# Optimization experiments

Hardware: AMD Instinct MI355X
Metric: run time of the kernel (lower is better)

Reference implementation:

```python
import jax, jax.numpy as jnp
import numpy as np

B, S, D, H = 2, 2048, 1024, 16
HD = D // H           # 64
AD = D // 8           # adapter dim 128


def setup_inputs() -> dict:
    key = jax.random.key(0)
    ks = jax.random.split(key, 16)
    s = 1.0 / np.sqrt(D)
    sa = 1.0 / np.sqrt(AD)
    return {
        "q": jax.random.normal(ks[0], (B, S, D), jnp.float32),
        "k": jax.random.normal(ks[1], (B, S, D), jnp.float32),
        "v": jax.random.normal(ks[2], (B, S, D), jnp.float32),
        "Wq": jax.random.normal(ks[3], (D, D), jnp.float32) * s,
        "bq": jnp.zeros((D,), jnp.float32),
        "Wk": jax.random.normal(ks[4], (D, D), jnp.float32) * s,
        "bk": jnp.zeros((D,), jnp.float32),
        "Wv": jax.random.normal(ks[5], (D, D), jnp.float32) * s,
        "bv": jnp.zeros((D,), jnp.float32),
        "Wo": jax.random.normal(ks[6], (D, D), jnp.float32) * s,
        "bo": jnp.zeros((D,), jnp.float32),
        "Wad": jax.random.normal(ks[7], (AD, D), jnp.float32) * s,
        "bad": jnp.zeros((AD,), jnp.float32),
        "Wau": jax.random.normal(ks[8], (D, AD), jnp.float32) * sa,
        "bau": jnp.zeros((D,), jnp.float32),
    }


def reference(q, k, v, Wq, bq, Wk, bk, Wv, bv, Wo, bo, Wad, bad, Wau, bau):
    # Linear projections (torch Linear: x @ W.T + b), split into heads
    def proj(x, W, b):
        y = jnp.einsum('bsd,ed->bse', x, W) + b
        return y.reshape(B, -1, H, HD).transpose(0, 2, 1, 3)  # [B,H,S,HD]

    qh, kh, vh = proj(q, Wq, bq), proj(k, Wk, bk), proj(v, Wv, bv)
    scores = jnp.einsum('bhqd,bhkd->bhqk', qh, kh) / np.sqrt(HD)  # [B,H,S,S]
    attn = jax.nn.softmax(scores, axis=-1)
    ctx = jnp.einsum('bhqk,bhkd->bhqd', attn, vh)
    ctx = ctx.transpose(0, 2, 1, 3).reshape(B, -1, D)  # [B,S,D]
    out = jnp.einsum('bsd,ed->bse', ctx, Wo) + bo
    # adapter: down -> GELU (exact erf) -> up, fused with residual
    a = jnp.einsum('bsd,ad->bsa', out, Wad) + bad
    a = jax.nn.gelu(a, approximate=False)
    a = jnp.einsum('bsa,da->bsd', a, Wau) + bau
    return out + a
```

## Files before the change

kernel.cpp:

```cpp
#include <hip/hip_runtime.h>
#include <hip/hip_bf16.h>
#include <math.h>

typedef __attribute__((ext_vector_type(8))) short short8;
typedef __attribute__((ext_vector_type(4))) float f32x4;

#define MFMA16(a,b,c) __builtin_amdgcn_mfma_f32_16x16x32_bf16((a),(b),(c),0,0,0)

__device__ __forceinline__ unsigned short f2bf(float f){
    union { __hip_bfloat16 b; unsigned short u; } cv;
    cv.b = __float2bfloat16(f);
    return cv.u;
}
__device__ __forceinline__ unsigned pk_bf16(float a, float b){
    unsigned r;
    asm("v_cvt_pk_bf16_f32 %0, %1, %2" : "=v"(r) : "v"(a), "v"(b));
    return r;
}
__device__ __forceinline__ float ex2(float x){
    return __builtin_amdgcn_exp2f(x);
}

#define GLD_LDS16(g, s) \
    __builtin_amdgcn_global_load_lds((const __attribute__((address_space(1))) void*)(g), \
                                     (__attribute__((address_space(3))) void*)(s), 16, 0, 0)

#define QSCALE 0.18033688011112042f
#define DEFER_THR 11.0f

struct CvtJobs {
    const float* src[9];
    unsigned short* dst[9];
    float scale[9];
    int n[9];
};

__global__ __launch_bounds__(256)
void convert_kernel(CvtJobs j, long long total4) {
    long long i4 = (long long)blockIdx.x * blockDim.x + threadIdx.x;
    if (i4 >= total4) return;
    long long rem = i4 * 4;
    int job = 0;
    while (job < 9 && rem >= j.n[job]) { rem -= j.n[job]; ++job; }
    if (job >= 9) return;
    const float sc = j.scale[job];
    const float4 v = *(const float4*)(j.src[job] + rem);
    ushort4 o;
    o.x = f2bf(v.x * sc); o.y = f2bf(v.y * sc);
    o.z = f2bf(v.z * sc); o.w = f2bf(v.w * sc);
    *(ushort4*)(j.dst[job] + rem) = o;
}

#define GEMM128_LOOP(Aptr, Bptr)                                                     \
    f32x4 acc[4][4] = {};                                                            \
    for (int k0 = 0; k0 < K; k0 += 32) {                                             \
        __syncthreads();                                                             \
        _Pragma("unroll")                                                            \
        for (int c = 0; c < 2; ++c) {                                                \
            const int id = c * 256 + tid;                                            \
            const int row = id >> 2, u = id & 3;                                     \
            const int su = u ^ ((row >> 1) & 3);                                     \
            GLD_LDS16((const char*)(Aptr) + ((size_t)(m0 + row) * K + k0) * 2 + su * 16, \
                      (char*)As + (c * 256 + w * 64) * 16);                          \
            GLD_LDS16((const char*)(Bptr) + ((size_t)(n0 + row) * K + k0) * 2 + su * 16, \
                      (char*)Bs + (c * 256 + w * 64) * 16);                          \
        }                                                                            \
        __syncthreads();                                                             \
        short8 af[4], bfr[4];                                                        \
        _Pragma("unroll")                                                            \
        for (int i = 0; i < 4; ++i)                                                  \
            af[i] = *(const short8*)((const char*)As + (wr * 64 + i * 16 + lr) * 64 + ru * 16); \
        _Pragma("unroll")                                                            \
        for (int jj = 0; jj < 4; ++jj)                                               \
            bfr[jj] = *(const short8*)((const char*)Bs + (wc * 64 + jj * 16 + lr) * 64 + ru * 16); \
        _Pragma("unroll")                                                            \
        for (int i = 0; i < 4; ++i)                                                  \
            _Pragma("unroll")                                                        \
            for (int jj = 0; jj < 4; ++jj)                                           \
                acc[i][jj] = MFMA16(af[i], bfr[jj], acc[i][jj]);                     \
    }

struct QKVArgs {
    const unsigned short* A[3];
    const unsigned short* W[3];
    const float* bias[3];
    float bscale[3];
    unsigned short* out[3];
};

__global__ __launch_bounds__(256)
void gemm_qkv(QKVArgs ar, int M, int N, int K)
{
    __shared__ unsigned short As[128 * 32];
    __shared__ unsigned short Bs[128 * 32];

    const int z = blockIdx.z;
    const unsigned short* A = ar.A[z];
    const unsigned short* W = ar.W[z];
    const int tid = threadIdx.x;
    const int w = tid >> 6, l = tid & 63;
    const int lr = l & 15, lg = l >> 4;
    const int wr = w >> 1, wc = w & 1;
    const int m0 = blockIdx.x * 128, n0 = blockIdx.y * 128;
    const int ru = lg ^ ((lr >> 1) & 3);

    GEMM128_LOOP(A, W)

    const float* bias = ar.bias[z];
    const float bsc = ar.bscale[z];
    unsigned short* out = ar.out[z];
    #pragma unroll
    for (int i = 0; i < 4; ++i)
        #pragma unroll
        for (int jj = 0; jj < 4; ++jj)
            #pragma unroll
            for (int r = 0; r < 4; ++r) {
                const int row = m0 + wr * 64 + i * 16 + lg * 4 + r;
                const int col = n0 + wc * 64 + jj * 16 + lr;
                const float c = acc[i][jj][r] + bias[col] * bsc;
                const int b = row >> 11, s = row & 2047, h = col >> 6, hd = col & 63;
                if (z < 2)
                    out[((((size_t)(b * 16 + h)) * 2048 + s) << 6) + hd] = f2bf(c);
                else
                    out[((((size_t)(b * 16 + h)) * 64 + hd) << 11) + s] = f2bf(c);
            }
}

template<int MODE>
__global__ __launch_bounds__(256)
void gemm_bf16(const unsigned short* __restrict__ A,
               const unsigned short* __restrict__ Wt,
               const float* __restrict__ bias,
               void* __restrict__ out0,
               void* __restrict__ out1,
               int M, int N, int K)
{
    __shared__ unsigned short As[128 * 32];
    __shared__ unsigned short Bs[128 * 32];

    const int tid = threadIdx.x;
    const int w = tid >> 6, l = tid & 63;
    const int lr = l & 15, lg = l >> 4;
    const int wr = w >> 1, wc = w & 1;
    const int m0 = blockIdx.x * 128, n0 = blockIdx.y * 128;
    const int ru = lg ^ ((lr >> 1) & 3);

    GEMM128_LOOP(A, Wt)

    #pragma unroll
    for (int i = 0; i < 4; ++i)
        #pragma unroll
        for (int jj = 0; jj < 4; ++jj)
            #pragma unroll
            for (int r = 0; r < 4; ++r) {
                const int row = m0 + wr * 64 + i * 16 + lg * 4 + r;
                const int col = n0 + wc * 64 + jj * 16 + lr;
                const float c = acc[i][jj][r] + bias[col];
                if (MODE == 2) {
                    ((float*)out0)[(size_t)row * N + col] = c;
                    ((unsigned short*)out1)[(size_t)row * N + col] = f2bf(c);
                } else {
                    ((float*)out0)[(size_t)row * N + col] =
                        c + ((const float*)out1)[(size_t)row * N + col];
                }
            }
}

__global__ __launch_bounds__(256)
void gemm64_gelu(const unsigned short* __restrict__ A,
                 const unsigned short* __restrict__ Wt,
                 const float* __restrict__ bias,
                 unsigned short* __restrict__ out,
                 int M, int N, int K)
{
    __shared__ unsigned short As[64 * 32];
    __shared__ unsigned short Bs[64 * 32];

    const int tid = threadIdx.x;
    const int w = tid >> 6, l = tid & 63;
    const int lr = l & 15, lg = l >> 4;
    const int wr = w >> 1, wc = w & 1;
    const int m0 = blockIdx.x * 64, n0 = blockIdx.y * 64;

    f32x4 acc[2][2] = {};

    for (int k0 = 0; k0 < K; k0 += 32) {
        const int row = tid >> 2, ch = tid & 3;
        __syncthreads();
        GLD_LDS16(A  + (size_t)(m0 + row) * K + k0 + ch * 8, As + (w * 64) * 8);
        GLD_LDS16(Wt + (size_t)(n0 + row) * K + k0 + ch * 8, Bs + (w * 64) * 8);
        __syncthreads();

        short8 af[2], bfr[2];
        #pragma unroll
        for (int i = 0; i < 2; ++i)
            af[i] = *(const short8*)(As + ((wr * 32 + i * 16 + lr) * 32 + lg * 8));
        #pragma unroll
        for (int jj = 0; jj < 2; ++jj)
            bfr[jj] = *(const short8*)(Bs + ((wc * 32 + jj * 16 + lr) * 32 + lg * 8));
        #pragma unroll
        for (int i = 0; i < 2; ++i)
            #pragma unroll
            for (int jj = 0; jj < 2; ++jj)
                acc[i][jj] = MFMA16(af[i], bfr[jj], acc[i][jj]);
    }

    #pragma unroll
    for (int i = 0; i < 2; ++i)
        #pragma unroll
        for (int jj = 0; jj < 2; ++jj)
            #pragma unroll
            for (int r = 0; r < 4; ++r) {
                const int row = m0 + wr * 32 + i * 16 + lg * 4 + r;
                const int col = n0 + wc * 32 + jj * 16 + lr;
                const float c = acc[i][jj][r] + bias[col];
                const float g = 0.5f * c * (1.0f + erff(c * 0.70710678118654752f));
                out[(size_t)row * N + col] = f2bf(g);
            }
}

__global__ __launch_bounds__(256)
void attn_mfma(const unsigned short* __restrict__ Qh,
               const unsigned short* __restrict__ Kh,
               const unsigned short* __restrict__ Vt,
               unsigned short* __restrict__ ctx)
{
    __shared__ unsigned short Ks[2][64 * 64];
    __shared__ unsigned short Vs[2][64 * 64];
    __shared__ unsigned short Ps[4][32 * 64];

    const int tid = threadIdx.x;
    const int w = tid >> 6, l = tid & 63;
    const int lr = l & 15, lg = l >> 4;

    const int p = blockIdx.x + blockIdx.y * 16;
    const int id = (p & 7) * 64 + (p >> 3);
    const int q0 = (id & 15) << 7;
    const int bh = id >> 4;

    const unsigned short* Qb = Qh + (size_t)bh * 131072;
    const char* Kb = (const char*)(Kh + (size_t)bh * 131072);
    const char* Vb = (const char*)(Vt + (size_t)bh * 131072);

    short8 qf[2][2];
    #pragma unroll
    for (int mm = 0; mm < 2; ++mm)
        #pragma unroll
        for (int c = 0; c < 2; ++c)
            qf[mm][c] = *(const short8*)(Qb + (size_t)(q0 + w * 32 + mm * 16 + lr) * 64
                                            + c * 32 + lg * 8);

    float mrow[2] = {-1e30f, -1e30f};
    float lrow[2] = {0.f, 0.f};
    f32x4 accO[2][4] = {};

    auto STAGE = [&](int bf, int kt) {
        #pragma unroll
        for (int c = 0; c < 2; ++c) {
            const int cid = c * 256 + tid;
            const int row = cid >> 3, u = cid & 7;
            const int su = u ^ (row & 7);
            GLD_LDS16(Kb + (size_t)(kt + row) * 128 + su * 16,
                      (char*)&Ks[bf][0] + (c * 256 + w * 64) * 16);
            GLD_LDS16(Vb + (size_t)row * 4096 + (size_t)kt * 2 + su * 16,
                      (char*)&Vs[bf][0] + (c * 256 + w * 64) * 16);
        }
    };

    STAGE(0, 0);
    __syncthreads();

    int cur = 0;
    for (int t = 0; t < 32; ++t) {
        if (t < 31) STAGE(cur ^ 1, (t + 1) * 64);

        const char* Kbuf = (const char*)&Ks[cur][0];
        const char* Vbuf = (const char*)&Vs[cur][0];

        f32x4 sf[2][4] = {};
        #pragma unroll
        for (int n = 0; n < 4; ++n) {
            const int krow = n * 16 + lr;
            const short8 kf0 = *(const short8*)(Kbuf + krow * 128 + ((0 * 4 + lg) ^ (lr & 7)) * 16);
            const short8 kf1 = *(const short8*)(Kbuf + krow * 128 + ((1 * 4 + lg) ^ (lr & 7)) * 16);
            #pragma unroll
            for (int mm = 0; mm < 2; ++mm) {
                sf[mm][n] = MFMA16(kf0, qf[mm][0], sf[mm][n]);
                sf[mm][n] = MFMA16(kf1, qf[mm][1], sf[mm][n]);
            }
        }

        short8 vf[4][2];
        #pragma unroll
        for (int n = 0; n < 4; ++n) {
            const int drow = n * 16 + lr;
            vf[n][0] = *(const short8*)(Vbuf + drow * 128 + ((0 * 4 + lg) ^ (lr & 7)) * 16);
            vf[n][1] = *(const short8*)(Vbuf + drow * 128 + ((1 * 4 + lg) ^ (lr & 7)) * 16);
        }

        float rm[2];
        bool need = false;
        #pragma unroll
        for (int mm = 0; mm < 2; ++mm) {
            float a = fmaxf(fmaxf(fmaxf(sf[mm][0][0], sf[mm][0][1]),
                                  fmaxf(sf[mm][0][2], sf[mm][0][3])),
                            fmaxf(fmaxf(sf[mm][1][0], sf[mm][1][1]),
                                  fmaxf(sf[mm][1][2], sf[mm][1][3])));
            float b = fmaxf(fmaxf(fmaxf(sf[mm][2][0], sf[mm][2][1]),
                                  fmaxf(sf[mm][2][2], sf[mm][2][3])),
                            fmaxf(fmaxf(sf[mm][3][0], sf[mm][3][1]),
                                  fmaxf(sf[mm][3][2], sf[mm][3][3])));
            float r2 = fmaxf(a, b);
            r2 = fmaxf(r2, __shfl_xor(r2, 16));
            r2 = fmaxf(r2, __shfl_xor(r2, 32));
            rm[mm] = r2;
            need |= (r2 > mrow[mm] + DEFER_THR);
        }
        if (__any(need)) {
            #pragma unroll
            for (int mm = 0; mm < 2; ++mm) {
                const float mnew = fmaxf(mrow[mm], rm[mm]);
                const float rsc = ex2(mrow[mm] - mnew);
                lrow[mm] *= rsc;
                mrow[mm] = mnew;
                #pragma unroll
                for (int r = 0; r < 4; ++r) {
                    const float rr = __shfl(rsc, (l & 48) | (lg * 4 + r));
                    #pragma unroll
                    for (int n = 0; n < 4; ++n) accO[mm][n][r] *= rr;
                }
            }
        }
        #pragma unroll
        for (int mm = 0; mm < 2; ++mm) {
            const float m = mrow[mm];
            float ls = lrow[mm];
            char* pbase = (char*)&Ps[w][0] + (mm * 16 + lr) * 128;
            #pragma unroll
            for (int n = 0; n < 4; ++n) {
                const float p0 = ex2(sf[mm][n][0] - m);
                const float p1 = ex2(sf[mm][n][1] - m);
                const float p2 = ex2(sf[mm][n][2] - m);
                const float p3 = ex2(sf[mm][n][3] - m);
                ls += (p0 + p1) + (p2 + p3);
                uint2 pk;
                pk.x = pk_bf16(p0, p1);
                pk.y = pk_bf16(p2, p3);
                *(uint2*)(pbase + (((n * 2 + (lg >> 1)) ^ (lr & 7)) * 16) + (lg & 1) * 8) = pk;
            }
            lrow[mm] = ls;
        }

        asm volatile("" ::: "memory");

        short8 pf[2][2];
        #pragma unroll
        for (int mm = 0; mm < 2; ++mm) {
            const char* pb = (const char*)&Ps[w][0] + (mm * 16 + lr) * 128;
            #pragma unroll
            for (int c = 0; c < 2; ++c) {
                union { uint2 q2[2]; short8 s8; } cvt;
                const char* base = pb + (((c * 4 + lg) ^ (lr & 7)) * 16);
                cvt.q2[0] = *(const uint2*)(base);
                cvt.q2[1] = *(const uint2*)(base + 8);
                pf[mm][c] = cvt.s8;
            }
        }

        #pragma unroll
        for (int n = 0; n < 4; ++n) {
            #pragma unroll
            for (int mm = 0; mm < 2; ++mm) {
                accO[mm][n] = MFMA16(pf[mm][0], vf[n][0], accO[mm][n]);
                accO[mm][n] = MFMA16(pf[mm][1], vf[n][1], accO[mm][n]);
            }
        }

        __syncthreads();
        cur ^= 1;
    }

    const int b = bh >> 4, h = bh & 15;
    #pragma unroll
    for (int mm = 0; mm < 2; ++mm) {
        float ls = lrow[mm];
        ls += __shfl_xor(ls, 16);
        ls += __shfl_xor(ls, 32);
        const float inv = 1.0f / ls;
        #pragma unroll
        for (int r = 0; r < 4; ++r) {
            const float vr = __shfl(inv, (l & 48) | (lg * 4 + r));
            const int srow = q0 + w * 32 + mm * 16 + lg * 4 + r;
            const size_t base = ((size_t)b * 2048 + srow) * 1024 + h * 64;
            #pragma unroll
            for (int n = 0; n < 4; ++n)
                ctx[base + n * 16 + lr] = f2bf(accO[mm][n][r] * vr);
        }
    }
}

extern "C" void kernel_launch(void* const* d_in, const int* in_sizes, int n_in,
                              void* d_out, int out_size, void* d_ws, size_t ws_size,
                              hipStream_t stream) {
    const float* q   = (const float*)d_in[0];
    const float* k   = (const float*)d_in[1];
    const float* v   = (const float*)d_in[2];
    const float* Wq  = (const float*)d_in[3];
    const float* bq  = (const float*)d_in[4];
    const float* Wk  = (const float*)d_in[5];
    const float* bk  = (const float*)d_in[6];
    const float* Wv  = (const float*)d_in[7];
    const float* bv  = (const float*)d_in[8];
    const float* Wo  = (const float*)d_in[9];
    const float* bo  = (const float*)d_in[10];
    const float* Wad = (const float*)d_in[11];
    const float* bad = (const float*)d_in[12];
    const float* Wau = (const float*)d_in[13];
    const float* bau = (const float*)d_in[14];

    const int M = 4096, D = 1024, AD = 128;
    const size_t SZ = (size_t)M * D;

    char* p = (char*)d_ws;
    size_t off = 0;
    auto alloc = [&](size_t bytes) { void* r = p + off; off = (off + bytes + 255) & ~(size_t)255; return r; };
    unsigned short* xq   = (unsigned short*)alloc(SZ * 2);
    unsigned short* xk   = (unsigned short*)alloc(SZ * 2);
    unsigned short* xv   = (unsigned short*)alloc(SZ * 2);
    unsigned short* Wqb  = (unsigned short*)alloc((size_t)D * D * 2);
    unsigned short* Wkb  = (unsigned short*)alloc((size_t)D * D * 2);
    unsigned short* Wvb  = (unsigned short*)alloc((size_t)D * D * 2);
    unsigned short* Wob  = (unsigned short*)alloc((size_t)D * D * 2);
    unsigned short* Wadb = (unsigned short*)alloc((size_t)AD * D * 2);
    unsigned short* Waub = (unsigned short*)alloc((size_t)D * AD * 2);
    unsigned short* Qh   = (unsigned short*)alloc(SZ * 2);
    unsigned short* Kh   = (unsigned short*)alloc(SZ * 2);
    unsigned short* Vt   = (unsigned short*)alloc(SZ * 2);
    unsigned short* ctx  = (unsigned short*)alloc(SZ * 2);
    float*          outp = (float*)alloc(SZ * 4);
    unsigned short* outb = (unsigned short*)alloc(SZ * 2);
    unsigned short* a1   = (unsigned short*)alloc((size_t)M * AD * 2);

    CvtJobs j;
    j.src[0] = q;   j.dst[0] = xq;   j.n[0] = (int)SZ;   j.scale[0] = 1.f;
    j.src[1] = k;   j.dst[1] = xk;   j.n[1] = (int)SZ;   j.scale[1] = 1.f;
    j.src[2] = v;   j.dst[2] = xv;   j.n[2] = (int)SZ;   j.scale[2] = 1.f;
    j.src[3] = Wq;  j.dst[3] = Wqb;  j.n[3] = D * D;     j.scale[3] = QSCALE;
    j.src[4] = Wk;  j.dst[4] = Wkb;  j.n[4] = D * D;     j.scale[4] = 1.f;
    j.src[5] = Wv;  j.dst[5] = Wvb;  j.n[5] = D * D;     j.scale[5] = 1.f;
    j.src[6] = Wo;  j.dst[6] = Wob;  j.n[6] = D * D;     j.scale[6] = 1.f;
    j.src[7] = Wad; j.dst[7] = Wadb; j.n[7] = AD * D;    j.scale[7] = 1.f;
    j.src[8] = Wau; j.dst[8] = Waub; j.n[8] = D * AD;    j.scale[8] = 1.f;
    long long total = 3LL * SZ + 4LL * D * D + 2LL * AD * D;
    long long total4 = total / 4;
    convert_kernel<<<dim3((unsigned)((total4 + 255) / 256)), dim3(256), 0, stream>>>(j, total4);

    const dim3 blk(256);

    QKVArgs qa;
    qa.A[0] = xq;  qa.A[1] = xk;  qa.A[2] = xv;
    qa.W[0] = Wqb; qa.W[1] = Wkb; qa.W[2] = Wvb;
    qa.bias[0] = bq; qa.bias[1] = bk; qa.bias[2] = bv;
    qa.bscale[0] = QSCALE; qa.bscale[1] = 1.f; qa.bscale[2] = 1.f;
    qa.out[0] = Qh; qa.out[1] = Kh; qa.out[2] = Vt;
    gemm_qkv<<<dim3(M / 128, D / 128, 3), blk, 0, stream>>>(qa, M, D, D);

    attn_mfma<<<dim3(2048 / 128, 32), blk, 0, stream>>>(Qh, Kh, Vt, ctx);

    gemm_bf16<2><<<dim3(M / 128, D / 128), blk, 0, stream>>>(ctx, Wob, bo, outp, outb, M, D, D);
    gemm64_gelu<<<dim3(M / 64, AD / 64), blk, 0, stream>>>(outb, Wadb, bad, a1, M, AD, D);
    gemm_bf16<4><<<dim3(M / 128, D / 128), blk, 0, stream>>>(a1, Waub, bau, d_out, outp, M, D, AD);
}
```

Before: 172.0 us.

## Halve attention query tile to 64 rows per block and add MFMA priority hints

The attention kernel now gives each block 64 query rows (16 per wave) instead of 128, doubling the grid to 1024 blocks, and shrinks the per-wave P scratch to match. The goal is more blocks in flight and lower register pressure, for better occupancy and latency hiding. It also wraps the MFMA sections in s_setprio hints. In exchange, each K/V tile loaded into LDS is reused across half as many query rows, so global/L2 traffic for K and V doubles.

```diff
diff --git a/kernel.cpp b/kernel.cpp
--- a/kernel.cpp
+++ b/kernel.cpp
@@ -227,32 +227,29 @@
 {
     __shared__ unsigned short Ks[2][64 * 64];
     __shared__ unsigned short Vs[2][64 * 64];
-    __shared__ unsigned short Ps[4][32 * 64];
+    __shared__ unsigned short Ps[4][16 * 64];
 
     const int tid = threadIdx.x;
     const int w = tid >> 6, l = tid & 63;
     const int lr = l & 15, lg = l >> 4;
 
-    const int p = blockIdx.x + blockIdx.y * 16;
-    const int id = (p & 7) * 64 + (p >> 3);
-    const int q0 = (id & 15) << 7;
-    const int bh = id >> 4;
+    const int p = blockIdx.x + blockIdx.y * 32;
+    const int id = (p & 7) * 128 + (p >> 3);
+    const int q0 = (id & 31) << 6;
+    const int bh = id >> 5;
 
     const unsigned short* Qb = Qh + (size_t)bh * 131072;
     const char* Kb = (const char*)(Kh + (size_t)bh * 131072);
     const char* Vb = (const char*)(Vt + (size_t)bh * 131072);
 
-    short8 qf[2][2];
+    short8 qf[2];
     #pragma unroll
-    for (int mm = 0; mm < 2; ++mm)
-        #pragma unroll
-        for (int c = 0; c < 2; ++c)
-            qf[mm][c] = *(const short8*)(Qb + (size_t)(q0 + w * 32 + mm * 16 + lr) * 64
-                                            + c * 32 + lg * 8);
-
-    float mrow[2] = {-1e30f, -1e30f};
-    float lrow[2] = {0.f, 0.f};
-    f32x4 accO[2][4] = {};
+    for (int c = 0; c < 2; ++c)
+        qf[c] = *(const short8*)(Qb + (size_t)(q0 + w * 16 + lr) * 64 + c * 32 + lg * 8);
+
+    float mrow = -1e30f;
+    float lrow = 0.f;
+    f32x4 accO[4] = {};
 
     auto STAGE = [&](int bf, int kt) {
         #pragma unroll
@@ -277,18 +274,17 @@
         const char* Kbuf = (const char*)&Ks[cur][0];
         const char* Vbuf = (const char*)&Vs[cur][0];
 
-        f32x4 sf[2][4] = {};
+        f32x4 sf[4] = {};
+        __builtin_amdgcn_s_setprio(1);
         #pragma unroll
         for (int n = 0; n < 4; ++n) {
             const int krow = n * 16 + lr;
             const short8 kf0 = *(const short8*)(Kbuf + krow * 128 + ((0 * 4 + lg) ^ (lr & 7)) * 16);
             const short8 kf1 = *(const short8*)(Kbuf + krow * 128 + ((1 * 4 + lg) ^ (lr & 7)) * 16);
-            #pragma unroll
-            for (int mm = 0; mm < 2; ++mm) {
-                sf[mm][n] = MFMA16(kf0, qf[mm][0], sf[mm][n]);
-                sf[mm][n] = MFMA16(kf1, qf[mm][1], sf[mm][n]);
-            }
-        }
+            sf[n] = MFMA16(kf0, qf[0], sf[n]);
+            sf[n] = MFMA16(kf1, qf[1], sf[n]);
+        }
+        __builtin_amdgcn_s_setprio(0);
 
         short8 vf[4][2];
         #pragma unroll
@@ -298,103 +294,86 @@
             vf[n][1] = *(const short8*)(Vbuf + drow * 128 + ((1 * 4 + lg) ^ (lr & 7)) * 16);
         }
 
-        float rm[2];
-        bool need = false;
-        #pragma unroll
-        for (int mm = 0; mm < 2; ++mm) {
-            float a = fmaxf(fmaxf(fmaxf(sf[mm][0][0], sf[mm][0][1]),
-                                  fmaxf(sf[mm][0][2], sf[mm][0][3])),
-                            fmaxf(fmaxf(sf[mm][1][0], sf[mm][1][1]),
-                                  fmaxf(sf[mm][1][2], sf[mm][1][3])));
-            float b = fmaxf(fmaxf(fmaxf(sf[mm][2][0], sf[mm][2][1]),
-                                  fmaxf(sf[mm][2][2], sf[mm][2][3])),
-                            fmaxf(fmaxf(sf[mm][3][0], sf[mm][3][1]),
-                                  fmaxf(sf[mm][3][2], sf[mm][3][3])));
-            float r2 = fmaxf(a, b);
-            r2 = fmaxf(r2, __shfl_xor(r2, 16));
-            r2 = fmaxf(r2, __shfl_xor(r2, 32));
-            rm[mm] = r2;
-            need |= (r2 > mrow[mm] + DEFER_THR);
-        }
+        float a = fmaxf(fmaxf(fmaxf(sf[0][0], sf[0][1]), fmaxf(sf[0][2], sf[0][3])),
+                        fmaxf(fmaxf(sf[1][0], sf[1][1]), fmaxf(sf[1][2], sf[1][3])));
+        float b2 = fmaxf(fmaxf(fmaxf(sf[2][0], sf[2][1]), fmaxf(sf[2][2], sf[2][3])),
+                         fmaxf(fmaxf(sf[3][0], sf[3][1]), fmaxf(sf[3][2], sf[3][3])));
+        float r2 = fmaxf(a, b2);
+        r2 = fmaxf(r2, __shfl_xor(r2, 16));
+        r2 = fmaxf(r2, __shfl_xor(r2, 32));
+        const bool need = (r2 > mrow + DEFER_THR);
         if (__any(need)) {
-            #pragma unroll
-            for (int mm = 0; mm < 2; ++mm) {
-                const float mnew = fmaxf(mrow[mm], rm[mm]);
-                const float rsc = ex2(mrow[mm] - mnew);
-                lrow[mm] *= rsc;
-                mrow[mm] = mnew;
+            const float mnew = fmaxf(mrow, r2);
+            const float rsc = ex2(mrow - mnew);
+            lrow *= rsc;
+            mrow = mnew;
+            #pragma unroll
+            for (int r = 0; r < 4; ++r) {
+                const float rr = __shfl(rsc, (l & 48) | (lg * 4 + r));
                 #pragma unroll
-                for (int r = 0; r < 4; ++r) {
-                    const float rr = __shfl(rsc, (l & 48) | (lg * 4 + r));
-                    #pragma unroll
-                    for (int n = 0; n < 4; ++n) accO[mm][n][r] *= rr;
-                }
-            }
-        }
-        #pragma unroll
-        for (int mm = 0; mm < 2; ++mm) {
-            const float m = mrow[mm];
-            float ls = lrow[mm];
-            char* pbase = (char*)&Ps[w][0] + (mm * 16 + lr) * 128;
+                for (int n = 0; n < 4; ++n) accO[n][r] *= rr;
+            }
+        }
+        {
+            const float m = mrow;
+            float ls = lrow;
+            char* pbase = (char*)&Ps[w][0] + lr * 128;
             #pragma unroll
             for (int n = 0; n < 4; ++n) {
-                const float p0 = ex2(sf[mm][n][0] - m);
-                const float p1 = ex2(sf[mm][n][1] - m);
-                const float p2 = ex2(sf[mm][n][2] - m);
-                const float p3 = ex2(sf[mm][n][3] - m);
+                const float p0 = ex2(sf[n][0] - m);
+                const float p1 = ex2(sf[n][1] - m);
+                const float p2 = ex2(sf[n][2] - m);
+                const float p3 = ex2(sf[n][3] - m);
                 ls += (p0 + p1) + (p2 + p3);
                 uint2 pk;
                 pk.x = pk_bf16(p0, p1);
                 pk.y = pk_bf16(p2, p3);
                 *(uint2*)(pbase + (((n * 2 + (lg >> 1)) ^ (lr & 7)) * 16) + (lg & 1) * 8) = pk;
             }
-            lrow[mm] = ls;
+            lrow = ls;
         }
 
         asm volatile("" ::: "memory");
 
-        short8 pf[2][2];
-        #pragma unroll
-        for (int mm = 0; mm < 2; ++mm) {
-            const char* pb = (const char*)&Ps[w][0] + (mm * 16 + lr) * 128;
+        short8 pf[2];
+        {
+            const char* pb = (const char*)&Ps[w][0] + lr * 128;
             #pragma unroll
             for (int c = 0; c < 2; ++c) {
                 union { uint2 q2[2]; short8 s8; } cvt;
                 const char* base = pb + (((c * 4 + lg) ^ (lr & 7)) * 16);
                 cvt.q2[0] = *(const uint2*)(base);
                 cvt.q2[1] = *(const uint2*)(base + 8);
-                pf[mm][c] = cvt.s8;
-            }
-        }
-
+                pf[c] = cvt.s8;
+            }
+        }
+
+        __builtin_amdgcn_s_setprio(1);
         #pragma unroll
         for (int n = 0; n < 4; ++n) {
-            #pragma unroll
-            for (int mm = 0; mm < 2; ++mm) {
-                accO[mm][n] = MFMA16(pf[mm][0], vf[n][0], accO[mm][n]);
-                accO[mm][n] = MFMA16(pf[mm][1], vf[n][1], accO[mm][n]);
-            }
-        }
+            accO[n] = MFMA16(pf[0], vf[n][0], accO[n]);
+            accO[n] = MFMA16(pf[1], vf[n][1], accO[n]);
+        }
+        __builtin_amdgcn_s_setprio(0);
 
         __syncthreads();
         cur ^= 1;
     }
 
     const int b = bh >> 4, h = bh & 15;
-    #pragma unroll
-    for (int mm = 0; mm < 2; ++mm) {
-        float ls = lrow[mm];
+    {
+        float ls = lrow;
         ls += __shfl_xor(ls, 16);
         ls += __shfl_xor(ls, 32);
         const float inv = 1.0f / ls;
         #pragma unroll
         for (int r = 0; r < 4; ++r) {
             const float vr = __shfl(inv, (l & 48) | (lg * 4 + r));
-            const int srow = q0 + w * 32 + mm * 16 + lg * 4 + r;
+            const int srow = q0 + w * 16 + lg * 4 + r;
             const size_t base = ((size_t)b * 2048 + srow) * 1024 + h * 64;
             #pragma unroll
             for (int n = 0; n < 4; ++n)
-                ctx[base + n * 16 + lr] = f2bf(accO[mm][n][r] * vr);
+                ctx[base + n * 16 + lr] = f2bf(accO[n][r] * vr);
         }
     }
 }
@@ -465,7 +444,7 @@
     qa.out[0] = Qh; qa.out[1] = Kh; qa.out[2] = Vt;
     gemm_qkv<<<dim3(M / 128, D / 128, 3), blk, 0, stream>>>(qa, M, D, D);
 
-    attn_mfma<<<dim3(2048 / 128, 32), blk, 0, stream>>>(Qh, Kh, Vt, ctx);
+    attn_mfma<<<dim3(32, 32), blk, 0, stream>>>(Qh, Kh, Vt, ctx);
 
     gemm_bf16<2><<<dim3(M / 128, D / 128), blk, 0, stream>>>(ctx, Wob, bo, outp, outb, M, D, D);
     gemm64_gelu<<<dim3(M / 64, AD / 64), blk, 0, stream>>>(outb, Wadb, bad, a1, M, AD, D);
```

Result: slower. 191.0 us (+11.1%).
